# Optimization experiments

Measured on AMD Instinct MI355X. Metric: run time of the kernel, lower is better.

The kernel has to match this reference:

```python
import jax, jax.numpy as jnp
import numpy as np

NUM_STEPS = 10
NUM_NODES = 100000
NUM_EDGES = 6400000


def setup_inputs() -> dict:
    key = jax.random.key(0)
    k1, k2, k3 = jax.random.split(key, 3)
    x = jax.random.uniform(k1, (NUM_NODES, 1), dtype=jnp.float32)
    edge_index = jax.random.randint(k2, (2, NUM_EDGES), 0, NUM_NODES, dtype=jnp.int64)
    edge_probs = jax.random.uniform(k3, (NUM_EDGES,), dtype=jnp.float32)
    # learned parameters (match torch init)
    time_decay = jnp.linspace(0.0, 1.0, NUM_STEPS, dtype=jnp.float32)
    node_bias = jnp.float32(0.0)
    edge_weight = jnp.ones((NUM_STEPS,), dtype=jnp.float32)
    return {
        "x": x,
        "edge_index": edge_index,
        "edge_probs": edge_probs,
        "time_decay": time_decay,
        "node_bias": node_bias,
        "edge_weight": edge_weight,
    }


def reference(x, edge_index, edge_probs, time_decay, node_bias, edge_weight):
    src, dst = edge_index[0], edge_index[1]
    num_nodes = x.shape[0]
    # per-step scalar scale: edge_weight[i] * exp(-time_decay[i]^2)
    step_scale = edge_weight * jnp.exp(-(time_decay ** 2))  # (num_steps,)

    def step(carry, scale):
        cur, surv = carry
        # gather node state to edges, scale, scatter-add back to nodes
        messages = cur[src] * (edge_probs[:, None] * scale)  # (num_edges, 1)
        cur = jax.ops.segment_sum(messages, dst, num_segments=num_nodes)
        cur = cur + node_bias
        surv = surv * (1.0 - cur)
        return (cur, surv), None

    (_, survival_prob), _ = jax.lax.scan(step, (x, 1.0 - x), step_scale)
    final_infection = 1.0 - survival_prob
    return jnp.clip(final_infection, 0.0, 1.0)
```

## Files before the change

### kernel.cpp

```cpp
#include <hip/hip_runtime.h>
#include <math.h>


#define MAXBINS     64
#define BIN_SHIFT   11
#define BIN_SIZE    2048
#define STAGE_CAP   64
#define BUCKET_GRID 768
#define BUCKET_TPB  256
#define BUCKET_K    8
#define STEP_TPB    256

__global__ void k_detect(const unsigned long long* ei, int* flag) {
    if (blockIdx.x == 0 && threadIdx.x == 0) {
        int is64 = 1;
        for (int k = 0; k < 64; ++k)
            if ((ei[k] >> 32) != 0ULL) { is64 = 0; break; }
        *flag = is64;
    }
}

__global__ void k_scales(const float* __restrict__ time_decay,
                         const float* __restrict__ edge_weight,
                         float* __restrict__ step_scale, int num_steps,
                         unsigned int* __restrict__ gcur) {
    int i = threadIdx.x;
    if (i < num_steps) {
        float td = time_decay[i];
        step_scale[i] = edge_weight[i] * expf(-td * td);
    }
    if (i < MAXBINS) gcur[i] = 0u;
}

__global__ void k_init(const float* __restrict__ x, float* __restrict__ cur0,
                       float* __restrict__ surv, int n) {
    int i = blockIdx.x * blockDim.x + threadIdx.x;
    if (i < n) {
        float v = x[i];
        cur0[i] = v;
        surv[i] = 1.0f - v;
    }
}

__global__ void k_bucket(const void* __restrict__ ei_raw, const int* __restrict__ flag,
                         const float* __restrict__ probs, unsigned int* __restrict__ gcur,
                         float2* __restrict__ sorted, unsigned int capr,
                         int E, int nbins) {
    __shared__ float2 buf[MAXBINS][STAGE_CAP];
    __shared__ unsigned int cnt[MAXBINS];
    __shared__ unsigned int gbase[MAXBINS];
    __shared__ unsigned int pref[MAXBINS + 1];
    const int t = threadIdx.x;
    const int is64 = *flag;
    const int chunk = (E + gridDim.x - 1) / gridDim.x;
    const int beg = blockIdx.x * chunk;
    const int end = min(E, beg + chunk);
    for (int i = t; i < nbins; i += BUCKET_TPB) cnt[i] = 0u;
    __syncthreads();
    const int ROUND = BUCKET_TPB * BUCKET_K;
    for (int rbeg = beg; rbeg < end; rbeg += ROUND) {
        for (int k = 0; k < BUCKET_K; ++k) {
            int e = rbeg + k * BUCKET_TPB + t;
            if (e < end) {
                int src, dst;
                if (is64) {
                    const long long* s = (const long long*)ei_raw;
                    src = (int)s[e]; dst = (int)s[e + E];
                } else {
                    const int* s = (const int*)ei_raw;
                    src = s[e]; dst = s[e + E];
                }
                float pr = probs[e];
                int bin = dst >> BIN_SHIFT;
                unsigned int payload = (unsigned int)src |
                                       ((unsigned int)(dst & (BIN_SIZE - 1)) << 17);
                unsigned int pos = atomicAdd(&cnt[bin], 1u);
                if (pos < STAGE_CAP) {
                    buf[bin][pos] = make_float2(__uint_as_float(payload), pr);
                } else {
                    unsigned int gp = atomicAdd(&gcur[bin], 1u);
                    if (gp < capr)
                        sorted[(size_t)bin * capr + gp] =
                            make_float2(__uint_as_float(payload), pr);
                }
            }
        }
        __syncthreads();
        if (t < 64) {
            unsigned int c = (t < nbins) ? min(cnt[t], (unsigned int)STAGE_CAP) : 0u;
            unsigned int inc = c;
            for (int off = 1; off < 64; off <<= 1) {
                unsigned int u = __shfl_up(inc, off, 64);
                if (t >= off) inc += u;
            }
            pref[t + 1] = inc;
            if (t == 0) pref[0] = 0u;
            if (t < nbins && c > 0u) gbase[t] = atomicAdd(&gcur[t], c);
        }
        __syncthreads();
        int total = (int)pref[nbins];
        for (int i = t; i < total; i += BUCKET_TPB) {
            int lo = 0, hi = nbins - 1;
            while (lo < hi) {
                int mid = (lo + hi + 1) >> 1;
                if ((int)pref[mid] <= i) lo = mid; else hi = mid - 1;
            }
            int idx = i - (int)pref[lo];
            unsigned int gp = gbase[lo] + (unsigned int)idx;
            if (gp < capr)
                sorted[(size_t)lo * capr + gp] = buf[lo][idx];
        }
        __syncthreads();
        for (int i = t; i < nbins; i += BUCKET_TPB) cnt[i] = 0u;
        __syncthreads();
    }
}

__global__ void k_step(const float2* __restrict__ sorted, const unsigned int* __restrict__ gcur,
                       const float* __restrict__ cur_in, float* __restrict__ part,
                       unsigned int capr, int pstride, int nbins, int splits) {
    __shared__ float acc[2][BIN_SIZE];
    const int bin = blockIdx.x / splits;
    const int sp  = blockIdx.x - bin * splits;
    const int t = threadIdx.x;
    float* accf = (float*)acc;
    for (int i = t; i < 2 * BIN_SIZE; i += STEP_TPB) accf[i] = 0.0f;
    __syncthreads();
    unsigned int cntv = min(gcur[bin], capr);
    unsigned int sub = (cntv + (unsigned int)splits - 1) / (unsigned int)splits;
    unsigned int s0 = min(cntv, (unsigned int)sp * sub);
    unsigned int s1 = min(cntv, s0 + sub);
    const float2* base = sorted + (size_t)bin * capr;
    for (unsigned int j = s0 + t; j < s1; j += STEP_TPB) {
        float2 kp = base[j];
        unsigned int v = __float_as_uint(kp.x);
        float m = cur_in[v & 0x1FFFFu] * kp.y;
        atomicAdd(&acc[t & 1][v >> 17], m);
    }
    __syncthreads();
    float* dst = part + (size_t)sp * pstride + (size_t)bin * BIN_SIZE;
    for (int i = t; i < BIN_SIZE; i += STEP_TPB)
        dst[i] = acc[0][i] + acc[1][i];
}

__global__ void k_reduce(const float* __restrict__ part, int pstride, int splits,
                         float* __restrict__ cur_out, float* __restrict__ surv,
                         const float* __restrict__ step_scale, const float* __restrict__ bias_p,
                         float* __restrict__ out, int step, int n, int last) {
    int i = blockIdx.x * blockDim.x + threadIdx.x;
    if (i >= n) return;
    float c = 0.0f;
    for (int s = 0; s < splits; ++s) c += part[(size_t)s * pstride + i];
    c = c * step_scale[step] + bias_p[0];
    if (!last) cur_out[i] = c;
    float sv = surv[i] * (1.0f - c);
    surv[i] = sv;
    if (last) out[i] = fminf(fmaxf(1.0f - sv, 0.0f), 1.0f);
}

__global__ void k_init0(const float* __restrict__ x, float* __restrict__ cur,
                        float* __restrict__ surv, float* __restrict__ acc, int n) {
    int i = blockIdx.x * blockDim.x + threadIdx.x;
    if (i < n) {
        float v = x[i];
        cur[i] = v; surv[i] = 1.0f - v; acc[i] = 0.0f;
    }
}

__global__ void k_edge_raw(const void* __restrict__ ei_raw, const int* __restrict__ flag,
                           const float* __restrict__ probs, const float* __restrict__ cur,
                           float* __restrict__ acc, const float* __restrict__ step_scale,
                           int step, int num_edges) {
    const float scale = step_scale[step];
    const int is64 = *flag;
    const int stride = gridDim.x * blockDim.x;
    for (int e = blockIdx.x * blockDim.x + threadIdx.x; e < num_edges; e += stride) {
        int src, dst;
        if (is64) {
            const long long* s = (const long long*)ei_raw;
            src = (int)s[e]; dst = (int)s[e + num_edges];
        } else {
            const int* s = (const int*)ei_raw;
            src = s[e]; dst = s[e + num_edges];
        }
        atomicAdd(&acc[dst], cur[src] * (probs[e] * scale));
    }
}

__global__ void k_node(float* __restrict__ cur, float* __restrict__ acc,
                       float* __restrict__ surv, const float* __restrict__ bias_p,
                       float* __restrict__ out, int n, int write_out) {
    int i = blockIdx.x * blockDim.x + threadIdx.x;
    if (i < n) {
        float c = acc[i] + bias_p[0];
        acc[i] = 0.0f;
        cur[i] = c;
        float s = surv[i] * (1.0f - c);
        surv[i] = s;
        if (write_out) out[i] = fminf(fmaxf(1.0f - s, 0.0f), 1.0f);
    }
}

static inline size_t al256(size_t x) { return (x + 255) & ~(size_t)255; }

extern "C" void kernel_launch(void* const* d_in, const int* in_sizes, int n_in,
                              void* d_out, int out_size, void* d_ws, size_t ws_size,
                              hipStream_t stream) {
    const float* x           = (const float*)d_in[0];
    const void*  ei          = d_in[1];
    const float* probs       = (const float*)d_in[2];
    const float* time_decay  = (const float*)d_in[3];
    const float* node_bias   = (const float*)d_in[4];
    const float* edge_weight = (const float*)d_in[5];
    float* outf = (float*)d_out;

    const int n = in_sizes[0];
    const int E = in_sizes[2];
    const int S = in_sizes[3];

    char* ws = (char*)d_ws;
    int*          flag       = (int*)ws;
    float*        step_scale = (float*)(ws + 64);
    unsigned int* gcur       = (unsigned int*)(ws + 256);

    const int nbins   = (n + BIN_SIZE - 1) >> BIN_SHIFT;
    const int pstride = nbins * BIN_SIZE;

    const double   meand  = (double)E / (nbins > 0 ? nbins : 1);
    const double   sigma  = sqrt(meand > 1.0 ? meand : 1.0);
    unsigned int   want   = (unsigned int)(meand + 16.0 * sigma + 64.0);
    unsigned int   least  = (unsigned int)(meand + 6.0 * sigma + 64.0);
    want  = (want  + 63u) & ~63u;
    least = (least + 63u) & ~63u;

    const size_t nbA      = al256((size_t)n * 4);
    const size_t off_buf  = 512;
    const size_t off_surv = off_buf + nbA;
    const size_t off_part = al256(off_surv + nbA);

    int splits = 0;
    unsigned int capr = 0;
    size_t off_sort = 0;
    const int cand[5] = {16, 12, 8, 6, 4};
    for (int ci = 0; ci < 5; ++ci) {
        int sp = cand[ci];
        size_t part_b = (size_t)sp * pstride * 4;
        size_t osort  = al256(off_part + part_b);
        if (ws_size <= osort) continue;
        size_t availb = ws_size - osort;
        unsigned int acap = (unsigned int)((availb / ((size_t)nbins * 8)) & ~(size_t)63);
        if (acap >= least) {
            splits  = sp;
            capr    = acap < want ? acap : want;
            off_sort = osort;
            break;
        }
    }

    const int nthreads  = 256;
    const int node_grid = (n + nthreads - 1) / nthreads;

    const bool ok = (n <= (1 << 17)) && (nbins >= 1) && (nbins <= MAXBINS) &&
                    (E > 0) && (splits > 0);

    k_detect<<<1, 64, 0, stream>>>((const unsigned long long*)ei, flag);
    k_scales<<<1, 64, 0, stream>>>(time_decay, edge_weight, step_scale, S, gcur);

    if (!ok) {
        float* cur  = (float*)(ws + off_buf);
        float* surv = (float*)(ws + off_surv);
        float* acc  = (float*)(ws + off_surv + nbA);
        k_init0<<<node_grid, nthreads, 0, stream>>>(x, cur, surv, acc, n);
        for (int s = 0; s < S; ++s) {
            k_edge_raw<<<2048, nthreads, 0, stream>>>(ei, flag, probs, cur, acc,
                                                      step_scale, s, E);
            k_node<<<node_grid, nthreads, 0, stream>>>(cur, acc, surv, node_bias,
                                                       outf, n, s == S - 1 ? 1 : 0);
        }
        return;
    }

    float*  bufA   = (float*)(ws + off_buf);
    float*  surv   = (float*)(ws + off_surv);
    float*  part   = (float*)(ws + off_part);
    float2* sorted = (float2*)(ws + off_sort);

    float* b0 = (S % 2 == 0) ? outf : bufA;
    float* b1 = (S % 2 == 0) ? bufA : outf;

    k_init<<<node_grid, nthreads, 0, stream>>>(x, b0, surv, n);

    k_bucket<<<BUCKET_GRID, BUCKET_TPB, 0, stream>>>(ei, flag, probs, gcur, sorted,
                                                     capr, E, nbins);

    const int step_grid = nbins * splits;
    for (int s = 0; s < S; ++s) {
        float* ci = (s % 2 == 0) ? b0 : b1;
        float* co = (s % 2 == 0) ? b1 : b0;
        k_step<<<step_grid, STEP_TPB, 0, stream>>>(sorted, gcur, ci, part,
                                                   capr, pstride, nbins, splits);
        k_reduce<<<node_grid, nthreads, 0, stream>>>(part, pstride, splits, co, surv,
                                                     step_scale, node_bias, outf,
                                                     s, n, s == S - 1 ? 1 : 0);
    }
}
```

Measured before the change: 686.2 us.

## Simplify bucket flush to per-wave copy and enlarge step blocks with 4-way accumulators

The bucket kernel's flush phase drops the prefix scan and per-element binary search, and instead assigns one wave per bin, with each lane copying one staged element. The step kernel moves to 1024-thread blocks with four shared-memory accumulator copies to spread LDS atomic contention. The split candidates are reduced so fewer partial buffers are written and summed, and the bucket grid grows. Larger step blocks raise LDS use per block (32KB) and may limit occupancy. Fewer splits also means fewer blocks per bin in the gather/scatter step.

```diff
diff --git a/kernel.cpp b/kernel.cpp
--- a/kernel.cpp
+++ b/kernel.cpp
@@ -6,10 +6,10 @@
 #define BIN_SHIFT   11
 #define BIN_SIZE    2048
 #define STAGE_CAP   64
-#define BUCKET_GRID 768
+#define BUCKET_GRID 1024
 #define BUCKET_TPB  256
 #define BUCKET_K    8
-#define STEP_TPB    256
+#define STEP_TPB    1024
 
 __global__ void k_detect(const unsigned long long* ei, int* flag) {
     if (blockIdx.x == 0 && threadIdx.x == 0) {
@@ -49,8 +49,9 @@
     __shared__ float2 buf[MAXBINS][STAGE_CAP];
     __shared__ unsigned int cnt[MAXBINS];
     __shared__ unsigned int gbase[MAXBINS];
-    __shared__ unsigned int pref[MAXBINS + 1];
     const int t = threadIdx.x;
+    const int wid = t >> 6, lane = t & 63;
+    const int nwaves = BUCKET_TPB / 64;
     const int is64 = *flag;
     const int chunk = (E + gridDim.x - 1) / gridDim.x;
     const int beg = blockIdx.x * chunk;
@@ -86,29 +87,18 @@
             }
         }
         __syncthreads();
-        if (t < 64) {
-            unsigned int c = (t < nbins) ? min(cnt[t], (unsigned int)STAGE_CAP) : 0u;
-            unsigned int inc = c;
-            for (int off = 1; off < 64; off <<= 1) {
-                unsigned int u = __shfl_up(inc, off, 64);
-                if (t >= off) inc += u;
+        if (t < nbins) {
+            unsigned int c = min(cnt[t], (unsigned int)STAGE_CAP);
+            if (c > 0u) gbase[t] = atomicAdd(&gcur[t], c);
+        }
+        __syncthreads();
+        for (int b = wid; b < nbins; b += nwaves) {
+            unsigned int c = min(cnt[b], (unsigned int)STAGE_CAP);
+            if ((unsigned int)lane < c) {
+                unsigned int gp = gbase[b] + (unsigned int)lane;
+                if (gp < capr)
+                    sorted[(size_t)b * capr + gp] = buf[b][lane];
             }
-            pref[t + 1] = inc;
-            if (t == 0) pref[0] = 0u;
-            if (t < nbins && c > 0u) gbase[t] = atomicAdd(&gcur[t], c);
-        }
-        __syncthreads();
-        int total = (int)pref[nbins];
-        for (int i = t; i < total; i += BUCKET_TPB) {
-            int lo = 0, hi = nbins - 1;
-            while (lo < hi) {
-                int mid = (lo + hi + 1) >> 1;
-                if ((int)pref[mid] <= i) lo = mid; else hi = mid - 1;
-            }
-            int idx = i - (int)pref[lo];
-            unsigned int gp = gbase[lo] + (unsigned int)idx;
-            if (gp < capr)
-                sorted[(size_t)lo * capr + gp] = buf[lo][idx];
         }
         __syncthreads();
         for (int i = t; i < nbins; i += BUCKET_TPB) cnt[i] = 0u;
@@ -116,15 +106,16 @@
     }
 }
 
-__global__ void k_step(const float2* __restrict__ sorted, const unsigned int* __restrict__ gcur,
-                       const float* __restrict__ cur_in, float* __restrict__ part,
-                       unsigned int capr, int pstride, int nbins, int splits) {
-    __shared__ float acc[2][BIN_SIZE];
+__global__ void __launch_bounds__(STEP_TPB)
+k_step(const float2* __restrict__ sorted, const unsigned int* __restrict__ gcur,
+       const float* __restrict__ cur_in, float* __restrict__ part,
+       unsigned int capr, int pstride, int nbins, int splits) {
+    __shared__ float acc[4][BIN_SIZE];
     const int bin = blockIdx.x / splits;
     const int sp  = blockIdx.x - bin * splits;
     const int t = threadIdx.x;
     float* accf = (float*)acc;
-    for (int i = t; i < 2 * BIN_SIZE; i += STEP_TPB) accf[i] = 0.0f;
+    for (int i = t; i < 4 * BIN_SIZE; i += STEP_TPB) accf[i] = 0.0f;
     __syncthreads();
     unsigned int cntv = min(gcur[bin], capr);
     unsigned int sub = (cntv + (unsigned int)splits - 1) / (unsigned int)splits;
@@ -135,12 +126,12 @@
         float2 kp = base[j];
         unsigned int v = __float_as_uint(kp.x);
         float m = cur_in[v & 0x1FFFFu] * kp.y;
-        atomicAdd(&acc[t & 1][v >> 17], m);
+        atomicAdd(&acc[t & 3][v >> 17], m);
     }
     __syncthreads();
     float* dst = part + (size_t)sp * pstride + (size_t)bin * BIN_SIZE;
     for (int i = t; i < BIN_SIZE; i += STEP_TPB)
-        dst[i] = acc[0][i] + acc[1][i];
+        dst[i] = acc[0][i] + acc[1][i] + acc[2][i] + acc[3][i];
 }
 
 __global__ void k_reduce(const float* __restrict__ part, int pstride, int splits,
@@ -241,8 +232,8 @@
     int splits = 0;
     unsigned int capr = 0;
     size_t off_sort = 0;
-    const int cand[5] = {16, 12, 8, 6, 4};
-    for (int ci = 0; ci < 5; ++ci) {
+    const int cand[4] = {8, 6, 5, 4};
+    for (int ci = 0; ci < 4; ++ci) {
         int sp = cand[ci];
         size_t part_b = (size_t)sp * pstride * 4;
         size_t osort  = al256(off_part + part_b);
```

Measured after the change: 682.0 us. Within noise of the previous version (-0.6%).
